# Kernel tuning notes

Hardware: AMD Instinct MI355X
Metric: run time of the kernel (lower is better)

## Reference

```python
import jax, jax.numpy as jnp
import numpy as np

M, B, U, D = 65536, 128, 256, 512
USAGE_DECAY = 0.95

def _l2n(x, axis):
    # tf.nn.l2_normalize semantics (K.l2_normalize)
    return x / jnp.sqrt(jnp.maximum(jnp.sum(x * x, axis=axis, keepdims=True), 1e-12))

def _lstm_cell(x, h, c, kernel, rec_kernel, bias):
    # Keras LSTMCell: gates in order i, f, c, o
    z = x @ kernel + h @ rec_kernel + bias  # [B, 4U]
    zi, zf, zc, zo = jnp.split(z, 4, axis=-1)
    i = jax.nn.sigmoid(zi)
    f = jax.nn.sigmoid(zf)
    c_new = f * c + i * jnp.tanh(zc)
    o = jax.nn.sigmoid(zo)
    h_new = o * jnp.tanh(c_new)
    return h_new, c_new

def setup_inputs() -> dict:
    key = jax.random.key(0)
    ks = jax.random.split(key, 10)
    return {
        "inputs": jax.random.normal(ks[0], (B, D), jnp.float32),
        "r_tm1": jnp.zeros((B, U), jnp.float32),
        "m_tm1": jax.random.uniform(ks[1], (M, U), jnp.float32),
        "c_wu_tm1": jax.random.uniform(ks[2], (M, B), jnp.float32),
        "c_wlu_tm1": jnp.zeros((M, B), jnp.float32),
        "c_wr_tm1": jax.random.uniform(ks[3], (M, B), jnp.float32),
        "h_tm1": jax.random.normal(ks[4], (B, U), jnp.float32) * 0.1,
        "cc_tm1": jax.random.normal(ks[5], (B, U), jnp.float32) * 0.1,
        "kernel": jax.random.normal(ks[6], (D + U, 4 * U), jnp.float32) * 0.02,
        "rec_kernel": jax.random.normal(ks[7], (U, 4 * U), jnp.float32) * 0.02,
        "bias": jnp.zeros((4 * U,), jnp.float32),
        "write_gate": jax.random.normal(ks[8], (1,), jnp.float32),
    }

def reference(inputs, r_tm1, m_tm1, c_wu_tm1, c_wlu_tm1, c_wr_tm1,
              h_tm1, cc_tm1, kernel, rec_kernel, bias, write_gate):
    # Controller step on [inputs, r_tm1]
    ctrl_in = jnp.concatenate([inputs, r_tm1], axis=1)          # [B, D+U]
    key_list, cc = _lstm_cell(ctrl_in, h_tm1, cc_tm1, kernel, rec_kernel, bias)  # [B, U]

    wg = jax.nn.sigmoid(write_gate)                              # [1]
    # NOTE: faithful to source -- scalar (1 - wg) is ADDED elementwise, then c_wlu added
    c_ww = wg * c_wr_tm1 + (1.0 - wg) + c_wlu_tm1                # [M, B]

    # cosine-similarity addressing
    cos = _l2n(key_list, 1) @ _l2n(m_tm1, 1).T                   # [B, M]
    # K.softmax on the transposed matrix => softmax over the BATCH axis (faithful)
    c_wr = jax.nn.softmax(cos.T, axis=-1)                        # [M, B]
    read = c_wr.T @ m_tm1                                        # [B, U]

    c_wu = USAGE_DECAY * c_wu_tm1 + c_wr + c_ww                  # [M, B]

    # top_k(c_wu.T, M): v.T[-1,:] is the per-batch minimum over slots
    mins = jnp.min(c_wu, axis=0)                                 # [B]
    min_idx = jnp.argmin(c_wu, axis=0)                           # [B]
    b_star = jnp.argmin(mins)                                    # scalar
    i_star = min_idx[b_star]                                     # global least-used slot

    c_wlu = (c_wu <= mins[None, :]).astype(jnp.float32)          # [M, B]

    # zeroing_matrix = one_hot(i_star broadcast to B cols, on=0, off=1) [M,B];
    # dot(zeroing[M,B], ones[B,U]) -> rows = B except zeroed row (faithful B scaling)
    keep = 1.0 - jax.nn.one_hot(i_star, M, dtype=jnp.float32)    # [M]
    memory = (float(B) * keep)[:, None] * m_tm1                  # [M, U]
    memory = c_ww @ key_list + memory                            # [M, U]

    return (read, memory, c_wu, c_wlu, c_wr, key_list, cc)
```

## Files before the change

kernel.cpp:

```cpp
#include <hip/hip_runtime.h>
#include <hip/hip_bf16.h>
#include <math.h>

#define NM 65536
#define NB 128
#define NU 256
#define ND 512

constexpr size_t OUT_READ = 0;
constexpr size_t OUT_MEM  = 32768;
constexpr size_t OUT_CWU  = OUT_MEM + 16777216;
constexpr size_t OUT_CWLU = OUT_CWU + 8388608;
constexpr size_t OUT_CWR  = OUT_CWLU + 8388608;
constexpr size_t OUT_KEY  = OUT_CWR + 8388608;
constexpr size_t OUT_CC   = OUT_KEY + 32768;

constexpr size_t WS_KLNT   = 0;
constexpr size_t WS_MINENC = 131072;
constexpr size_t WS_MINS   = 132096;
constexpr size_t WS_ISTAR  = 132608;
constexpr size_t WS_PART   = 135168;

typedef __attribute__((ext_vector_type(8))) short short8v;
typedef __attribute__((ext_vector_type(4))) float floatx4;

__device__ __forceinline__ unsigned fenc(float x) {
    unsigned u = __float_as_uint(x);
    return (u & 0x80000000u) ? ~u : (u | 0x80000000u);
}
__device__ __forceinline__ float fdec(unsigned e) {
    unsigned u = (e & 0x80000000u) ? (e ^ 0x80000000u) : ~e;
    return __uint_as_float(u);
}
__device__ __forceinline__ float sigm(float x) { return 1.0f / (1.0f + expf(-x)); }
__device__ __forceinline__ unsigned short f2b(float f) {
    __hip_bfloat16 h = __float2bfloat16(f);
    return *reinterpret_cast<unsigned short*>(&h);
}

__global__ __launch_bounds__(256) void k_lstm(
    const float* __restrict__ xin_g, const float* __restrict__ r_tm1,
    const float* __restrict__ h_tm1, const float* __restrict__ cc_tm1,
    const float* __restrict__ Wk, const float* __restrict__ Wr,
    const float* __restrict__ bias, float* __restrict__ out,
    float* __restrict__ klnT, unsigned long long* __restrict__ minenc)
{
    const int b = blockIdx.x, t = threadIdx.x;
    __shared__ float xin[ND + NU];
    __shared__ float hh[NU];
    __shared__ float red[NU];
    for (int k = t; k < ND; k += 256) xin[k] = xin_g[b * ND + k];
    xin[ND + t] = r_tm1[b * NU + t];
    hh[t] = h_tm1[b * NU + t];
    out[OUT_READ + b * NU + t] = 0.f;
    if (b == 0 && t < NB) minenc[t] = ~0ULL;
    __syncthreads();

    float zi = bias[t], zf = bias[NU + t], zc = bias[2 * NU + t], zo = bias[3 * NU + t];
    #pragma unroll 4
    for (int k = 0; k < ND + NU; ++k) {
        const float x = xin[k];
        const float* w = Wk + (size_t)k * (4 * NU);
        zi += x * w[t]; zf += x * w[NU + t]; zc += x * w[2 * NU + t]; zo += x * w[3 * NU + t];
    }
    #pragma unroll 4
    for (int k = 0; k < NU; ++k) {
        const float x = hh[k];
        const float* w = Wr + (size_t)k * (4 * NU);
        zi += x * w[t]; zf += x * w[NU + t]; zc += x * w[2 * NU + t]; zo += x * w[3 * NU + t];
    }
    const float gi = sigm(zi), gf = sigm(zf), gc = tanhf(zc), go = sigm(zo);
    const float cold = cc_tm1[b * NU + t];
    const float cn = __fadd_rn(__fmul_rn(gf, cold), __fmul_rn(gi, gc));
    const float hn = __fmul_rn(go, tanhf(cn));
    out[OUT_KEY + b * NU + t] = hn;
    out[OUT_CC + b * NU + t] = cn;
    red[t] = hn * hn;
    __syncthreads();
    for (int s = 128; s > 0; s >>= 1) { if (t < s) red[t] += red[t + s]; __syncthreads(); }
    const float nrm = sqrtf(fmaxf(red[0], 1e-12f));
    klnT[t * NB + b] = hn / nrm;
}

__global__ __launch_bounds__(256, 2) void k_dot(
    const float* __restrict__ mT, const float* __restrict__ klnT,
    const float* __restrict__ cwr_t, const float* __restrict__ cwlu_t,
    const float* __restrict__ cwu_t, const float* __restrict__ wgp,
    float* __restrict__ out, unsigned long long* __restrict__ minenc)
{
    __shared__ float smem[16384];
    __shared__ float rn_s[128];
    const int t = threadIdx.x, w = t >> 6, l = t & 63;
    const int tx = t & 15, ty = t >> 4;
    const int b0a = tx * 4, b0b = 64 + tx * 4;
    const int s0 = ty * 8;
    const int sb = blockIdx.x * 128;

    #pragma unroll 4
    for (int i = 0; i < 32; ++i) {
        const int s = w * 32 + i;
        const float4 mv = *(const float4*)(mT + (size_t)(sb + s) * NU + l * 4);
        float ss = mv.x * mv.x + mv.y * mv.y + mv.z * mv.z + mv.w * mv.w;
        #pragma unroll
        for (int d = 1; d < 64; d <<= 1) ss += __shfl_xor(ss, d);
        if (l == 0) rn_s[s] = sqrtf(fmaxf(ss, 1e-12f));
    }

    const int sl = t & 127, ug = t >> 7;
    const int ku_ = t >> 4, kb = (t & 15) * 4;

    float acc[8][8];
    #pragma unroll
    for (int i = 0; i < 8; ++i)
        #pragma unroll
        for (int j = 0; j < 8; ++j) acc[i][j] = 0.f;

    float4 gm[2], gk[2];
    #pragma unroll
    for (int i = 0; i < 2; ++i) {
        gm[i] = *(const float4*)(mT + (size_t)(sb + sl) * NU + (ug + 2 * i) * 4);
        gk[i] = *(const float4*)(klnT + (size_t)ku_ * NB + kb + i * 64);
    }
    for (int c = 0; c < 16; ++c) {
        const int mo = (c & 1) * 2048;
        const int ko = 4096 + (c & 1) * 2048;
        #pragma unroll
        for (int i = 0; i < 2; ++i) {
            const int uo = (ug + 2 * i) * 4;
            smem[mo + (uo + 0) * 128 + sl] = gm[i].x;
            smem[mo + (uo + 1) * 128 + sl] = gm[i].y;
            smem[mo + (uo + 2) * 128 + sl] = gm[i].z;
            smem[mo + (uo + 3) * 128 + sl] = gm[i].w;
            *(float4*)&smem[ko + ku_ * 128 + kb + i * 64] = gk[i];
        }
        __syncthreads();
        if (c < 15) {
            const int uc = (c + 1) * 16;
            #pragma unroll
            for (int i = 0; i < 2; ++i) {
                gm[i] = *(const float4*)(mT + (size_t)(sb + sl) * NU + uc + (ug + 2 * i) * 4);
                gk[i] = *(const float4*)(klnT + (size_t)(uc + ku_) * NB + kb + i * 64);
            }
        }
        #pragma unroll 4
        for (int u = 0; u < 16; ++u) {
            const float4 sv0 = *(const float4*)&smem[mo + u * 128 + s0];
            const float4 sv1 = *(const float4*)&smem[mo + u * 128 + s0 + 4];
            const float4 kv0 = *(const float4*)&smem[ko + u * 128 + b0a];
            const float4 kv1 = *(const float4*)&smem[ko + u * 128 + b0b];
            const float sv[8] = {sv0.x, sv0.y, sv0.z, sv0.w, sv1.x, sv1.y, sv1.z, sv1.w};
            const float kv[8] = {kv0.x, kv0.y, kv0.z, kv0.w, kv1.x, kv1.y, kv1.z, kv1.w};
            #pragma unroll
            for (int i = 0; i < 8; ++i)
                #pragma unroll
                for (int j = 0; j < 8; ++j)
                    acc[i][j] += sv[i] * kv[j];
        }
        __syncthreads();
    }

    #pragma unroll
    for (int i = 0; i < 8; ++i) {
        *(float4*)&smem[(s0 + i) * 128 + b0a] = make_float4(acc[i][0], acc[i][1], acc[i][2], acc[i][3]);
        *(float4*)&smem[(s0 + i) * 128 + b0b] = make_float4(acc[i][4], acc[i][5], acc[i][6], acc[i][7]);
    }
    __syncthreads();

    const float wg = sigm(wgp[0]);
    const float omw = __fsub_rn(1.f, wg);
    unsigned long long lmin0 = ~0ULL, lmin1 = ~0ULL;
    #pragma unroll 2
    for (int i = 0; i < 32; ++i) {
        const int s = w * 32 + i;
        const int m = sb + s;
        const float2 dv = *(const float2*)&smem[s * 128 + 2 * l];
        const float rnv = rn_s[s];
        const float2 wrt = ((const float2*)(cwr_t + (size_t)m * NB))[l];
        const float2 wlu = ((const float2*)(cwlu_t + (size_t)m * NB))[l];
        const float2 wut = ((const float2*)(cwu_t + (size_t)m * NB))[l];
        const float c0 = dv.x / rnv, c1 = dv.y / rnv;
        float mx = fmaxf(c0, c1);
        #pragma unroll
        for (int d = 1; d < 64; d <<= 1) mx = fmaxf(mx, __shfl_xor(mx, d));
        const float e0 = expf(c0 - mx), e1 = expf(c1 - mx);
        float sm = e0 + e1;
        #pragma unroll
        for (int d = 1; d < 64; d <<= 1) sm += __shfl_xor(sm, d);
        const float w0 = e0 / sm, w1 = e1 / sm;
        const float cww0 = __fadd_rn(__fadd_rn(__fmul_rn(wg, wrt.x), omw), wlu.x);
        const float cww1 = __fadd_rn(__fadd_rn(__fmul_rn(wg, wrt.y), omw), wlu.y);
        const float cu0 = __fadd_rn(__fadd_rn(__fmul_rn(0.95f, wut.x), w0), cww0);
        const float cu1 = __fadd_rn(__fadd_rn(__fmul_rn(0.95f, wut.y), w1), cww1);
        ((float2*)(out + OUT_CWR))[(size_t)m * 64 + l] = make_float2(w0, w1);
        ((float2*)(out + OUT_CWU))[(size_t)m * 64 + l] = make_float2(cu0, cu1);
        const unsigned long long e0u = (((unsigned long long)fenc(cu0)) << 32) | (unsigned)m;
        const unsigned long long e1u = (((unsigned long long)fenc(cu1)) << 32) | (unsigned)m;
        lmin0 = (e0u < lmin0) ? e0u : lmin0;
        lmin1 = (e1u < lmin1) ? e1u : lmin1;
    }
    atomicMin(&minenc[2 * l], lmin0);
    atomicMin(&minenc[2 * l + 1], lmin1);
}

__global__ void k_argmin(const unsigned long long* __restrict__ minenc,
                         float* __restrict__ mins, unsigned* __restrict__ istar)
{
    __shared__ unsigned long long red[NB];
    const int t = threadIdx.x;
    const unsigned long long e = minenc[t];
    const unsigned enc32 = (unsigned)(e >> 32);
    mins[t] = fdec(enc32);
    red[t] = (((unsigned long long)enc32) << 32) | (unsigned)t;
    __syncthreads();
    for (int s = 64; s > 0; s >>= 1) {
        if (t < s) { const unsigned long long o = red[t + s]; if (o < red[t]) red[t] = o; }
        __syncthreads();
    }
    if (t == 0) {
        const unsigned bstar = (unsigned)(red[0] & 0xFFFFFFFFu);
        istar[0] = (unsigned)(minenc[bstar] & 0xFFFFFFFFu);
    }
}

__global__ __launch_bounds__(256, 2) void k_mem(
    const float* __restrict__ mT,
    const float* __restrict__ cwr_t, const float* __restrict__ cwlu_t,
    const float* __restrict__ wgp, const float* __restrict__ mins,
    const unsigned* __restrict__ istar_p, float* __restrict__ out)
{
    __shared__ unsigned short cwwb[128 * 136];
    __shared__ unsigned short keyT[128 * 136];
    const int t = threadIdx.x, w = t >> 6, l = t & 63;
    const int sb = blockIdx.x * 128;
    const float wg = sigm(wgp[0]);
    const float omw = __fsub_rn(1.f, wg);
    const int istar = (int)istar_p[0];

    {
        const int srow = t >> 5;
        const int bc = (t & 31) * 4;
        for (int it = 0; it < 16; ++it) {
            const int s = it * 8 + srow;
            const size_t row = (size_t)(sb + s) * NB + bc;
            const float4 wr = *(const float4*)(cwr_t + row);
            const float4 lu = *(const float4*)(cwlu_t + row);
            const float4 wu = *(const float4*)(out + OUT_CWU + row);
            float4 cw;
            cw.x = __fadd_rn(__fadd_rn(__fmul_rn(wg, wr.x), omw), lu.x);
            cw.y = __fadd_rn(__fadd_rn(__fmul_rn(wg, wr.y), omw), lu.y);
            cw.z = __fadd_rn(__fadd_rn(__fmul_rn(wg, wr.z), omw), lu.z);
            cw.w = __fadd_rn(__fadd_rn(__fmul_rn(wg, wr.w), omw), lu.w);
            ushort4 pk;
            pk.x = f2b(cw.x); pk.y = f2b(cw.y); pk.z = f2b(cw.z); pk.w = f2b(cw.w);
            *(ushort4*)&cwwb[s * 136 + bc] = pk;
            const float4 mb = *(const float4*)(mins + bc);
            float4 wl;
            wl.x = (wu.x <= mb.x) ? 1.f : 0.f;
            wl.y = (wu.y <= mb.y) ? 1.f : 0.f;
            wl.z = (wu.z <= mb.z) ? 1.f : 0.f;
            wl.w = (wu.w <= mb.w) ? 1.f : 0.f;
            *(float4*)(out + OUT_CWLU + row) = wl;
        }
    }

    const int rk = (l >> 4) * 8;
    const int rr = l & 15;

    for (int uh = 0; uh < 2; ++uh) {
        if (uh) __syncthreads();
        {
            const int br = t >> 5;
            const int ko = (t & 31) * 4;
            for (int it = 0; it < 16; ++it) {
                const int b = it * 8 + br;
                const float4 kv = *(const float4*)(out + OUT_KEY + (size_t)b * NU + uh * 128 + ko);
                keyT[(ko + 0) * 136 + b] = f2b(kv.x);
                keyT[(ko + 1) * 136 + b] = f2b(kv.y);
                keyT[(ko + 2) * 136 + b] = f2b(kv.z);
                keyT[(ko + 3) * 136 + b] = f2b(kv.w);
            }
        }
        __syncthreads();

        floatx4 acc0[8], acc1[8];
        #pragma unroll
        for (int ut = 0; ut < 8; ++ut) {
            acc0[ut] = (floatx4){0.f, 0.f, 0.f, 0.f};
            acc1[ut] = (floatx4){0.f, 0.f, 0.f, 0.f};
        }
        #pragma unroll
        for (int kc = 0; kc < 4; ++kc) {
            const short8v a0 = *(const short8v*)&cwwb[(w * 32 + rr) * 136 + kc * 32 + rk];
            const short8v a1 = *(const short8v*)&cwwb[(w * 32 + 16 + rr) * 136 + kc * 32 + rk];
            #pragma unroll
            for (int ut = 0; ut < 8; ++ut) {
                const short8v bf = *(const short8v*)&keyT[(ut * 16 + rr) * 136 + kc * 32 + rk];
                acc0[ut] = __builtin_amdgcn_mfma_f32_16x16x32_bf16(a0, bf, acc0[ut], 0, 0, 0);
                acc1[ut] = __builtin_amdgcn_mfma_f32_16x16x32_bf16(a1, bf, acc1[ut], 0, 0, 0);
            }
        }

        #pragma unroll
        for (int ut = 0; ut < 8; ++ut) {
            const int gcol = uh * 128 + ut * 16 + rr;
            #pragma unroll
            for (int q = 0; q < 4; ++q) {
                const int grow0 = sb + w * 32 + (l >> 4) * 4 + q;
                const int grow1 = grow0 + 16;
                const float mv0 = mT[(size_t)grow0 * NU + gcol];
                const float mv1 = mT[(size_t)grow1 * NU + gcol];
                const float kf0 = (grow0 == istar) ? 0.f : 128.f;
                const float kf1 = (grow1 == istar) ? 0.f : 128.f;
                out[OUT_MEM + (size_t)grow0 * NU + gcol] = acc0[ut][q] + kf0 * mv0;
                out[OUT_MEM + (size_t)grow1 * NU + gcol] = acc1[ut][q] + kf1 * mv1;
            }
        }
    }
}

template <int USE_PART>
__global__ __launch_bounds__(256) void k_read(
    const float* __restrict__ mT, float* __restrict__ out, float* __restrict__ part)
{
    const int t = threadIdx.x, w = t >> 6, l = t & 63;
    const int r = blockIdx.x, ri = r >> 1, uh = r & 1;
    const int rk = (l >> 4) * 8, rr = l & 15;
    const float* cwr = out + OUT_CWR;

    floatx4 acc[2][8];
    #pragma unroll
    for (int bt = 0; bt < 2; ++bt)
        #pragma unroll
        for (int ut = 0; ut < 8; ++ut) acc[bt][ut] = (floatx4){0.f, 0.f, 0.f, 0.f};

    for (int c = 0; c < 8; ++c) {
        const size_t m0 = (size_t)(ri * 256 + c * 32 + rk);
        short8v a[2];
        #pragma unroll
        for (int bt = 0; bt < 2; ++bt) {
            const float* ap = cwr + m0 * NB + w * 32 + bt * 16 + rr;
            #pragma unroll
            for (int i = 0; i < 8; ++i) a[bt][i] = (short)f2b(ap[i * NB]);
        }
        short8v bf[8];
        #pragma unroll
        for (int ut = 0; ut < 8; ++ut) {
            const float* bp = mT + m0 * NU + uh * 128 + ut * 16 + rr;
            #pragma unroll
            for (int i = 0; i < 8; ++i) bf[ut][i] = (short)f2b(bp[i * NU]);
        }
        #pragma unroll
        for (int bt = 0; bt < 2; ++bt)
            #pragma unroll
            for (int ut = 0; ut < 8; ++ut)
                acc[bt][ut] = __builtin_amdgcn_mfma_f32_16x16x32_bf16(a[bt], bf[ut], acc[bt][ut], 0, 0, 0);
    }

    if (USE_PART) {
        float* dst = part + (size_t)r * (128 * 128);
        #pragma unroll
        for (int bt = 0; bt < 2; ++bt)
            #pragma unroll
            for (int ut = 0; ut < 8; ++ut)
                #pragma unroll
                for (int q = 0; q < 4; ++q)
                    dst[(size_t)(w * 32 + bt * 16 + (l >> 4) * 4 + q) * 128 + ut * 16 + rr] = acc[bt][ut][q];
    } else {
        #pragma unroll
        for (int bt = 0; bt < 2; ++bt)
            #pragma unroll
            for (int ut = 0; ut < 8; ++ut)
                #pragma unroll
                for (int q = 0; q < 4; ++q)
                    atomicAdd(out + OUT_READ + (size_t)(w * 32 + bt * 16 + (l >> 4) * 4 + q) * NU
                                  + uh * 128 + ut * 16 + rr, acc[bt][ut][q]);
    }
}

__global__ __launch_bounds__(256) void k_redread(const float* __restrict__ part,
                                                 float* __restrict__ out)
{
    const int b = blockIdx.x, u = threadIdx.x;
    const int uh = u >> 7, ul = u & 127;
    float s = 0.f;
    #pragma unroll 4
    for (int ri = 0; ri < 256; ++ri)
        s += part[((size_t)(ri * 2 + uh) * 128 + b) * 128 + ul];
    out[OUT_READ + b * NU + u] = s;
}

extern "C" void kernel_launch(void* const* d_in, const int* in_sizes, int n_in,
                              void* d_out, int out_size, void* d_ws, size_t ws_size,
                              hipStream_t stream)
{
    const float* inputs    = (const float*)d_in[0];
    const float* r_tm1     = (const float*)d_in[1];
    const float* m_tm1     = (const float*)d_in[2];
    const float* c_wu_tm1  = (const float*)d_in[3];
    const float* c_wlu_tm1 = (const float*)d_in[4];
    const float* c_wr_tm1  = (const float*)d_in[5];
    const float* h_tm1     = (const float*)d_in[6];
    const float* cc_tm1    = (const float*)d_in[7];
    const float* Wk        = (const float*)d_in[8];
    const float* Wr        = (const float*)d_in[9];
    const float* bias      = (const float*)d_in[10];
    const float* wgate     = (const float*)d_in[11];
    float* out = (float*)d_out;
    char* ws = (char*)d_ws;

    float* klnT = (float*)(ws + WS_KLNT);
    unsigned long long* minenc = (unsigned long long*)(ws + WS_MINENC);
    float* mins = (float*)(ws + WS_MINS);
    unsigned* istar = (unsigned*)(ws + WS_ISTAR);
    float* part = (float*)(ws + WS_PART);
    const bool use_part = ws_size >= WS_PART + (size_t)512 * 128 * 128 * 4;

    hipLaunchKernelGGL(k_lstm, dim3(128), dim3(256), 0, stream,
                       inputs, r_tm1, h_tm1, cc_tm1, Wk, Wr, bias, out, klnT, minenc);
    hipLaunchKernelGGL(k_dot, dim3(512), dim3(256), 0, stream,
                       m_tm1, klnT, c_wr_tm1, c_wlu_tm1, c_wu_tm1, wgate, out, minenc);
    hipLaunchKernelGGL(k_argmin, dim3(1), dim3(128), 0, stream, minenc, mins, istar);
    hipLaunchKernelGGL(k_mem, dim3(512), dim3(256), 0, stream,
                       m_tm1, c_wr_tm1, c_wlu_tm1, wgate, mins, istar, out);
    if (use_part) {
        hipLaunchKernelGGL((k_read<1>), dim3(512), dim3(256), 0, stream, m_tm1, out, part);
        hipLaunchKernelGGL(k_redread, dim3(128), dim3(256), 0, stream, part, out);
    } else {
        hipLaunchKernelGGL((k_read<0>), dim3(512), dim3(256), 0, stream, m_tm1, out, part);
    }
}
```

Before: 401.9 us.

## Stage read operands through LDS and vectorize memory-update epilogue via LDS transpose

k_read previously gathered each MFMA operand element with strided scalar global loads. It now loads cwr and memory tiles with coalesced float4 reads, converts them to bf16, and stores them transposed in shared memory before the MFMA loop. The k_mem epilogue now writes accumulators to an LDS scratch area that reuses keyT, then does float4 reads of m_tm1 and float4 writes of the memory output instead of scattered scalar accesses. Both changes aim to cut uncoalesced global traffic, at the cost of extra LDS use, barriers and possible bank conflicts.

```diff
diff --git a/kernel.cpp b/kernel.cpp
--- a/kernel.cpp
+++ b/kernel.cpp
@@ -228,8 +228,8 @@
     const float* __restrict__ wgp, const float* __restrict__ mins,
     const unsigned* __restrict__ istar_p, float* __restrict__ out)
 {
-    __shared__ unsigned short cwwb[128 * 136];
-    __shared__ unsigned short keyT[128 * 136];
+    __shared__ alignas(16) unsigned short cwwb[128 * 136];
+    __shared__ alignas(16) unsigned short keyT[128 * 136];
     const int t = threadIdx.x, w = t >> 6, l = t & 63;
     const int sb = blockIdx.x * 128;
     const float wg = sigm(wgp[0]);
@@ -300,19 +300,29 @@
             }
         }
 
-        #pragma unroll
-        for (int ut = 0; ut < 8; ++ut) {
-            const int gcol = uh * 128 + ut * 16 + rr;
-            #pragma unroll
-            for (int q = 0; q < 4; ++q) {
-                const int grow0 = sb + w * 32 + (l >> 4) * 4 + q;
-                const int grow1 = grow0 + 16;
-                const float mv0 = mT[(size_t)grow0 * NU + gcol];
-                const float mv1 = mT[(size_t)grow1 * NU + gcol];
-                const float kf0 = (grow0 == istar) ? 0.f : 128.f;
-                const float kf1 = (grow1 == istar) ? 0.f : 128.f;
-                out[OUT_MEM + (size_t)grow0 * NU + gcol] = acc0[ut][q] + kf0 * mv0;
-                out[OUT_MEM + (size_t)grow1 * NU + gcol] = acc1[ut][q] + kf1 * mv1;
+        __syncthreads();
+        float* scr = (float*)keyT + w * 2112;
+        const int erow = l >> 2, ecb = (l & 3) * 4;
+        #pragma unroll
+        for (int bt = 0; bt < 2; ++bt) {
+            #pragma unroll
+            for (int ut = 0; ut < 8; ++ut)
+                #pragma unroll
+                for (int q = 0; q < 4; ++q)
+                    scr[((l >> 4) * 4 + q) * 132 + ut * 16 + rr] =
+                        (bt == 0) ? acc0[ut][q] : acc1[ut][q];
+            const int gs = sb + w * 32 + bt * 16 + erow;
+            const float kf = (gs == istar) ? 0.f : 128.f;
+            #pragma unroll
+            for (int j = 0; j < 8; ++j) {
+                const float4 d = *(const float4*)&scr[erow * 132 + j * 16 + ecb];
+                const float4 mv = *(const float4*)(mT + (size_t)gs * NU + uh * 128 + j * 16 + ecb);
+                float4 o;
+                o.x = d.x + kf * mv.x;
+                o.y = d.y + kf * mv.y;
+                o.z = d.z + kf * mv.z;
+                o.w = d.w + kf * mv.w;
+                *(float4*)(out + OUT_MEM + (size_t)gs * NU + uh * 128 + j * 16 + ecb) = o;
             }
         }
     }
@@ -322,10 +332,13 @@
 __global__ __launch_bounds__(256) void k_read(
     const float* __restrict__ mT, float* __restrict__ out, float* __restrict__ part)
 {
+    __shared__ alignas(16) unsigned short cwrb[128 * 40];
+    __shared__ alignas(16) unsigned short mb[128 * 40];
     const int t = threadIdx.x, w = t >> 6, l = t & 63;
     const int r = blockIdx.x, ri = r >> 1, uh = r & 1;
     const int rk = (l >> 4) * 8, rr = l & 15;
     const float* cwr = out + OUT_CWR;
+    const int srow = t >> 3, sc = (t & 7) * 16;
 
     floatx4 acc[2][8];
     #pragma unroll
@@ -334,26 +347,30 @@
         for (int ut = 0; ut < 8; ++ut) acc[bt][ut] = (floatx4){0.f, 0.f, 0.f, 0.f};
 
     for (int c = 0; c < 8; ++c) {
-        const size_t m0 = (size_t)(ri * 256 + c * 32 + rk);
-        short8v a[2];
-        #pragma unroll
-        for (int bt = 0; bt < 2; ++bt) {
-            const float* ap = cwr + m0 * NB + w * 32 + bt * 16 + rr;
-            #pragma unroll
-            for (int i = 0; i < 8; ++i) a[bt][i] = (short)f2b(ap[i * NB]);
-        }
-        short8v bf[8];
+        const size_t m0 = (size_t)(ri * 256 + c * 32);
+        #pragma unroll
+        for (int q = 0; q < 4; ++q) {
+            const float4 v = *(const float4*)(cwr + (m0 + srow) * NB + sc + q * 4);
+            cwrb[(sc + q * 4 + 0) * 40 + srow] = f2b(v.x);
+            cwrb[(sc + q * 4 + 1) * 40 + srow] = f2b(v.y);
+            cwrb[(sc + q * 4 + 2) * 40 + srow] = f2b(v.z);
+            cwrb[(sc + q * 4 + 3) * 40 + srow] = f2b(v.w);
+            const float4 u = *(const float4*)(mT + (m0 + srow) * NU + uh * 128 + sc + q * 4);
+            mb[(sc + q * 4 + 0) * 40 + srow] = f2b(u.x);
+            mb[(sc + q * 4 + 1) * 40 + srow] = f2b(u.y);
+            mb[(sc + q * 4 + 2) * 40 + srow] = f2b(u.z);
+            mb[(sc + q * 4 + 3) * 40 + srow] = f2b(u.w);
+        }
+        __syncthreads();
+        const short8v a0 = *(const short8v*)&cwrb[(w * 32 + rr) * 40 + rk];
+        const short8v a1 = *(const short8v*)&cwrb[(w * 32 + 16 + rr) * 40 + rk];
         #pragma unroll
         for (int ut = 0; ut < 8; ++ut) {
-            const float* bp = mT + m0 * NU + uh * 128 + ut * 16 + rr;
-            #pragma unroll
-            for (int i = 0; i < 8; ++i) bf[ut][i] = (short)f2b(bp[i * NU]);
-        }
-        #pragma unroll
-        for (int bt = 0; bt < 2; ++bt)
-            #pragma unroll
-            for (int ut = 0; ut < 8; ++ut)
-                acc[bt][ut] = __builtin_amdgcn_mfma_f32_16x16x32_bf16(a[bt], bf[ut], acc[bt][ut], 0, 0, 0);
+            const short8v bf = *(const short8v*)&mb[(ut * 16 + rr) * 40 + rk];
+            acc[0][ut] = __builtin_amdgcn_mfma_f32_16x16x32_bf16(a0, bf, acc[0][ut], 0, 0, 0);
+            acc[1][ut] = __builtin_amdgcn_mfma_f32_16x16x32_bf16(a1, bf, acc[1][ut], 0, 0, 0);
+        }
+        __syncthreads();
     }
 
     if (USE_PART) {
```

After: 400.9 us (median of 2 runs). Within noise of the previous version (-0.3%).
